# Kernel optimization log

Hardware: AMD Instinct MI355X
Metric: run time of the kernel (lower is better)

Reference implementation:

```python
import jax, jax.numpy as jnp
import numpy as np

D_MODEL = 1024
N_HEADS = 16
D_HEAD = D_MODEL // N_HEADS


def setup_inputs() -> dict:
    key = jax.random.key(0)
    ks = jax.random.split(key, 9)
    s = 1.0 / np.sqrt(D_MODEL)
    def lin(kw, kb):
        W = jax.random.uniform(kw, (D_MODEL, D_MODEL), jnp.float32, -s, s)
        b = jax.random.uniform(kb, (D_MODEL,), jnp.float32, -s, s)
        return W, b
    Wq, bq = lin(ks[0], ks[1])
    Wk, bk = lin(ks[2], ks[3])
    Wv, bv = lin(ks[4], ks[5])
    Wo, bo = lin(ks[6], ks[7])
    x = jax.random.normal(ks[8], (4, 2048, D_MODEL), jnp.float32)
    return {"x": x, "Wq": Wq, "bq": bq, "Wk": Wk, "bk": bk,
            "Wv": Wv, "bv": bv, "Wo": Wo, "bo": bo}


def reference(x, Wq, bq, Wk, bk, Wv, bv, Wo, bo):
    B, T, C = x.shape
    # torch Linear: y = x @ W.T + b
    Q = x @ Wq.T + bq
    K = x @ Wk.T + bk
    V = x @ Wv.T + bv
    # [B, H, T, Dh]
    Q = Q.reshape(B, T, N_HEADS, D_HEAD).transpose(0, 2, 1, 3)
    K = K.reshape(B, T, N_HEADS, D_HEAD).transpose(0, 2, 1, 3)
    V = V.reshape(B, T, N_HEADS, D_HEAD).transpose(0, 2, 1, 3)
    scale = jnp.float32(np.sqrt(D_HEAD))
    scores = jnp.einsum('bhqd,bhkd->bhqk', Q, K) / scale
    causal = jnp.tril(jnp.ones((T, T), dtype=bool))  # True where allowed
    scores = jnp.where(causal, scores, jnp.float32(-jnp.inf))
    attn = jax.nn.softmax(scores, axis=-1)
    out = jnp.einsum('bhqk,bhkd->bhqd', attn, V)
    out = out.transpose(0, 2, 1, 3).reshape(B, T, C)
    return out @ Wo.T + bo
```

## Files before the change

### kernel.cpp

```cpp
#include <hip/hip_runtime.h>
#include <hip/hip_bf16.h>


typedef float f32x4 __attribute__((ext_vector_type(4)));
typedef __bf16 bf16x8 __attribute__((ext_vector_type(8)));

#define DEVI __device__ __forceinline__

#define QSCALE 0.1803368801111204f

template<int N> struct IC { static constexpr int value = N; };

DEVI ushort f2b(float x) {
  __hip_bfloat16 h = __float2bfloat16(x);
  return __builtin_bit_cast(ushort, h);
}

DEVI unsigned int pkbf(float a, float b) {
#if __has_builtin(__builtin_amdgcn_cvt_pk_bf16_f32)
  typedef __bf16 bf16x2 __attribute__((ext_vector_type(2)));
  bf16x2 r = __builtin_amdgcn_cvt_pk_bf16_f32(a, b);
  return __builtin_bit_cast(unsigned int, r);
#else
  return (unsigned int)f2b(a) | ((unsigned int)f2b(b) << 16);
#endif
}

DEVI bf16x8 ldsFrag(const ushort* p) {
  return __builtin_bit_cast(bf16x8, *(const uint4*)p);
}

DEVI f32x4 mfma16(bf16x8 a, bf16x8 b, f32x4 c) {
  return __builtin_amdgcn_mfma_f32_16x16x32_bf16(a, b, c, 0, 0, 0);
}

DEVI void gload_lds16(const ushort* g, ushort* l) {
  __builtin_amdgcn_global_load_lds(
      (const __attribute__((address_space(1))) unsigned int*)g,
      (__attribute__((address_space(3))) unsigned int*)l, 16, 0, 0);
}

__global__ void k_cvt(const float4* __restrict__ in, ushort4* __restrict__ out, int n4) {
  int i = blockIdx.x * 256 + threadIdx.x;
  if (i >= n4) return;
  float4 f = in[i];
  ushort4 o;
  o.x = f2b(f.x); o.y = f2b(f.y); o.z = f2b(f.z); o.w = f2b(f.w);
  out[i] = o;
}

__global__ void k_cvtW(const float4* __restrict__ w0, const float4* __restrict__ w1,
                       const float4* __restrict__ w2, const float4* __restrict__ w3,
                       ushort4* __restrict__ out) {
  const int y = blockIdx.y;
  const float4* src = (y == 0) ? w0 : (y == 1) ? w1 : (y == 2) ? w2 : w3;
  const int i = blockIdx.x * 256 + threadIdx.x;
  float4 f = src[i];
  ushort4 o;
  o.x = f2b(f.x); o.y = f2b(f.y); o.z = f2b(f.z); o.w = f2b(f.w);
  out[y * 262144 + i] = o;
}

template<int MODE>
__global__ __launch_bounds__(256)
void k_gemm(const ushort* __restrict__ A, const ushort* __restrict__ W,
            const float* __restrict__ b0, const float* __restrict__ b1,
            const float* __restrict__ b2, float* __restrict__ outF,
            ushort* __restrict__ oQ, ushort* __restrict__ oK, ushort* __restrict__ oV) {
  __shared__ ushort As[128 * 64];
  __shared__ ushort Bs[128 * 64];
  const int tid = threadIdx.x;
  const int wave = tid >> 6, lane = tid & 63;
  const int col = lane & 15, quad = lane >> 4;
  const int id = blockIdx.x;
  const int s_ = id >> 3;
  const int m0 = ((id & 7) * 8 + (s_ & 7)) * 128;
  const int n0 = (s_ >> 3) * 128;
  const int wm = (wave >> 1) * 64, wn = (wave & 1) * 64;
  f32x4 acc[4][4] = {};

  const int grow = lane >> 3;
  const int gchunk = ((lane & 7) ^ grow) * 8;
  const ushort* Ag = A + (size_t)(m0 + wave * 8 + grow) * 1024 + gchunk;
  const ushort* Wg = W + (size_t)(n0 + wave * 8 + grow) * 1024 + gchunk;
  ushort* AsW = &As[wave * 512];
  ushort* BsW = &Bs[wave * 512];

  const int matId = (MODE == 0) ? (n0 >> 10) : 0;
  const int cswz = col & 7;

  auto kloop = [&](auto swc) {
    constexpr bool SW = (decltype(swc)::value != 0);
    for (int k0 = 0; k0 < 1024; k0 += 64) {
      __syncthreads();
#pragma unroll
      for (int g = 0; g < 4; ++g) {
        gload_lds16(Ag + (size_t)g * 32 * 1024 + k0, AsW + g * 2048);
        gload_lds16(Wg + (size_t)g * 32 * 1024 + k0, BsW + g * 2048);
      }
      __syncthreads();
#pragma unroll
      for (int kk = 0; kk < 2; ++kk) {
        bf16x8 af[4], bfr[4];
#pragma unroll
        for (int i = 0; i < 4; ++i)
          af[i] = ldsFrag(&As[(wm + i * 16 + col) * 64 + (((kk * 4 + quad) ^ cswz) * 8)]);
#pragma unroll
        for (int j = 0; j < 4; ++j)
          bfr[j] = ldsFrag(&Bs[(wn + j * 16 + col) * 64 + (((kk * 4 + quad) ^ cswz) * 8)]);
#pragma unroll
        for (int i = 0; i < 4; ++i)
#pragma unroll
          for (int j = 0; j < 4; ++j) {
            if constexpr (SW)
              acc[i][j] = mfma16(bfr[j], af[i], acc[i][j]);
            else
              acc[i][j] = mfma16(af[i], bfr[j], acc[i][j]);
          }
      }
    }
  };

  if (MODE == 1 || matId < 2) kloop(IC<1>{}); else kloop(IC<0>{});

  if (MODE == 1) {
#pragma unroll
    for (int j = 0; j < 4; ++j) {
      const int nb = n0 + wn + j * 16 + quad * 4;
      const float4 bb = *(const float4*)&b0[nb];
#pragma unroll
      for (int i = 0; i < 4; ++i) {
        const int m = m0 + wm + i * 16 + col;
        float4 v;
        v.x = acc[i][j][0] + bb.x;
        v.y = acc[i][j][1] + bb.y;
        v.z = acc[i][j][2] + bb.z;
        v.w = acc[i][j][3] + bb.w;
        *(float4*)&outF[(size_t)m * 1024 + nb] = v;
      }
    }
  } else if (matId < 2) {
    ushort* dst = (matId == 0) ? oQ : oK;
    const float* bias = (matId == 0) ? b0 : b1;
    const float sc = (matId == 0) ? QSCALE : 1.0f;
#pragma unroll
    for (int j = 0; j < 4; ++j) {
      const int nl = ((n0 & 1023) + wn + j * 16 + quad * 4);
      const int h = nl >> 6, dh0 = nl & 63;
      const float4 bb = *(const float4*)&bias[nl];
#pragma unroll
      for (int i = 0; i < 4; ++i) {
        const int m = m0 + wm + i * 16 + col;
        const int b = m >> 11, t = m & 2047;
        ushort4 pk;
        pk.x = f2b((acc[i][j][0] + bb.x) * sc);
        pk.y = f2b((acc[i][j][1] + bb.y) * sc);
        pk.z = f2b((acc[i][j][2] + bb.z) * sc);
        pk.w = f2b((acc[i][j][3] + bb.w) * sc);
        *(ushort4*)&dst[(((size_t)(b * 16 + h) * 2048) + t) * 64 + dh0] = pk;
      }
    }
  } else {
#pragma unroll
    for (int j = 0; j < 4; ++j) {
      const int nl = ((n0 & 1023) + wn + j * 16 + col);
      const int h = nl >> 6, dh = nl & 63;
      const float bn = b2[nl];
#pragma unroll
      for (int i = 0; i < 4; ++i) {
        const int mBase = m0 + wm + i * 16 + quad * 4;
        const int b = mBase >> 11, t = mBase & 2047;
        ushort4 pk;
        pk.x = f2b(acc[i][j][0] + bn);
        pk.y = f2b(acc[i][j][1] + bn);
        pk.z = f2b(acc[i][j][2] + bn);
        pk.w = f2b(acc[i][j][3] + bn);
        *(ushort4*)&oV[(((size_t)(b * 16 + h) * 64) + dh) * 2048 + t] = pk;
      }
    }
  }
}

__global__ __launch_bounds__(256, 3)
void k_attn(const ushort* __restrict__ Q, const ushort* __restrict__ K,
            const ushort* __restrict__ Vt, ushort* __restrict__ AO) {
  __shared__ ushort Ks[2 * 4096];
  __shared__ ushort Vs[2 * 4096];
  __shared__ ushort Os[512];
  __shared__ ushort Ps[4 * 2 * 16 * 72];
  const int tid = threadIdx.x;
  const int wave = tid >> 6, lane = tid & 63;
  const int col = lane & 15, quad = lane >> 4;
  const int id = blockIdx.x;
  const int bh = (id & 7) * 8 + ((id >> 3) & 7);
  const int tt = id >> 6;
  const int hi = tt >> 2, lo = tt & 3;
  const int t = (hi & 1) ? (15 - (hi >> 1) - 2 * lo) : ((hi >> 1) + 2 * lo);
  const int q0 = t * 128;
  const ushort* Qg = Q + (size_t)bh * 2048 * 64;
  const ushort* Kg = K + (size_t)bh * 2048 * 64;
  const ushort* Vg = Vt + (size_t)bh * 64 * 2048;

  if (tid < 128) {
    const ushort one = 0x3F80;
    ushort4 zv;
    if (tid < 8) { zv.x = one; zv.y = one; zv.z = one; zv.w = one; }
    else         { zv.x = 0;   zv.y = 0;   zv.z = 0;   zv.w = 0;   }
    *(ushort4*)&Os[tid * 4] = zv;
  }

  bf16x8 qf[2][2];
#pragma unroll
  for (int s = 0; s < 2; ++s) {
    const ushort* p = Qg + (q0 + wave * 32 + s * 16 + col) * 64 + quad * 8;
    qf[s][0] = __builtin_bit_cast(bf16x8, *(const uint4*)p);
    qf[s][1] = __builtin_bit_cast(bf16x8, *(const uint4*)(p + 32));
  }

  f32x4 o[2][4] = {};
  f32x4 la[2] = {};

  const int grow = lane >> 3;
  const int gchunk = ((lane & 7) ^ grow) * 8;
  const ushort* kPtr = Kg + (wave * 8 + grow) * 64 + gchunk;
  const ushort* vPtr = Vg + (size_t)(wave * 8 + grow) * 2048 + gchunk;
  ushort* Pw0 = &Ps[((wave * 2 + 0) * 16 + col) * 72];
  ushort* Pw1 = &Ps[((wave * 2 + 1) * 16 + col) * 72];
  const int cswz = col & 7;

  auto stage = [&](auto bufc) {
    constexpr int BUF = decltype(bufc)::value;
    ushort* kb = &Ks[BUF * 4096 + wave * 512];
    ushort* vb = &Vs[BUF * 4096 + wave * 512];
    gload_lds16(kPtr,             kb);
    gload_lds16(kPtr + 32 * 64,   kb + 2048);
    gload_lds16(vPtr,             vb);
    gload_lds16(vPtr + 32 * 2048, vb + 2048);
    kPtr += 64 * 64;
    vPtr += 64;
  };

  auto step = [&](auto bufc, auto maskc, int j0) {
    constexpr int BUF = decltype(bufc)::value;
    constexpr bool MASKED = (decltype(maskc)::value != 0);
    const ushort* Kb = &Ks[BUF * 4096];
    const ushort* Vb = &Vs[BUF * 4096];
    bf16x8 kf[4][2];
#pragma unroll
    for (int i = 0; i < 4; ++i) {
      kf[i][0] = ldsFrag(&Kb[(i * 16 + col) * 64 + (((0 * 4 + quad) ^ cswz) * 8)]);
      kf[i][1] = ldsFrag(&Kb[(i * 16 + col) * 64 + (((1 * 4 + quad) ^ cswz) * 8)]);
    }
#pragma unroll
    for (int s = 0; s < 2; ++s) {
      ushort* Pw = s ? Pw1 : Pw0;
      const int dlim = MASKED ? (q0 + wave * 32 + s * 16 + col - j0 - quad * 4) : 0;
#pragma unroll
      for (int i = 0; i < 4; ++i) {
        f32x4 z = {0.f, 0.f, 0.f, 0.f};
        f32x4 sv = mfma16(kf[i][0], qf[s][0], z);
        sv = mfma16(kf[i][1], qf[s][1], sv);
        if (MASKED) {
#pragma unroll
          for (int r = 0; r < 4; ++r)
            if (i * 16 + r > dlim) sv[r] = -1e30f;
        }
        f32x4 pv;
#pragma unroll
        for (int r = 0; r < 4; ++r) pv[r] = __builtin_amdgcn_exp2f(sv[r]);
        uint2 pk;
        pk.x = pkbf(pv[0], pv[1]);
        pk.y = pkbf(pv[2], pv[3]);
        *(uint2*)&Pw[i * 16 + quad * 4] = pk;
      }
    }
    bf16x8 osf = ldsFrag(&Os[col * 32 + quad * 8]);
#pragma unroll
    for (int c = 0; c < 2; ++c) {
      bf16x8 pb0 = ldsFrag(&Pw0[c * 32 + quad * 8]);
      bf16x8 pb1 = ldsFrag(&Pw1[c * 32 + quad * 8]);
      la[0] = mfma16(osf, pb0, la[0]);
      la[1] = mfma16(osf, pb1, la[1]);
#pragma unroll
      for (int i = 0; i < 4; ++i) {
        bf16x8 vf = ldsFrag(&Vb[(i * 16 + col) * 64 + (((c * 4 + quad) ^ cswz) * 8)]);
        o[0][i] = mfma16(vf, pb0, o[0][i]);
        o[1][i] = mfma16(vf, pb1, o[1][i]);
      }
    }
  };

  __syncthreads();
  stage(IC<0>{});
  for (int it2 = 0; it2 < t; ++it2) {
    __syncthreads();
    stage(IC<1>{});
    step(IC<0>{}, IC<0>{}, 0);
    __syncthreads();
    stage(IC<0>{});
    step(IC<1>{}, IC<0>{}, 0);
  }
  __syncthreads();
  stage(IC<1>{});
  step(IC<0>{}, IC<1>{}, q0);
  __syncthreads();
  step(IC<1>{}, IC<1>{}, q0 + 64);

  const float invs[2] = {1.0f / __shfl(la[0][0], col), 1.0f / __shfl(la[1][0], col)};
  const int b = bh >> 4, h = bh & 15;
#pragma unroll
  for (int s = 0; s < 2; ++s) {
    const float inv = invs[s];
    const int tq = q0 + wave * 32 + s * 16 + col;
    ushort* dst = AO + (size_t)(b * 2048 + tq) * 1024 + h * 64;
#pragma unroll
    for (int i = 0; i < 4; ++i) {
      f32x4 v = o[s][i];
      ushort4 pk;
      pk.x = f2b(v[0] * inv);
      pk.y = f2b(v[1] * inv);
      pk.z = f2b(v[2] * inv);
      pk.w = f2b(v[3] * inv);
      *(ushort4*)&dst[i * 16 + quad * 4] = pk;
    }
  }
}

extern "C" void kernel_launch(void* const* d_in, const int* in_sizes, int n_in,
                              void* d_out, int out_size, void* d_ws, size_t ws_size,
                              hipStream_t stream) {
  const float* x  = (const float*)d_in[0];
  const float* Wq = (const float*)d_in[1];
  const float* bq = (const float*)d_in[2];
  const float* Wk = (const float*)d_in[3];
  const float* bk = (const float*)d_in[4];
  const float* Wv = (const float*)d_in[5];
  const float* bv = (const float*)d_in[6];
  const float* Wo = (const float*)d_in[7];
  const float* bo = (const float*)d_in[8];
  float* out = (float*)d_out;

  char* ws = (char*)d_ws;
  ushort* xb    = (ushort*)ws;
  ushort* Wcat  = (ushort*)(ws + (size_t)16 * 1024 * 1024);
  ushort* Wob   = Wcat + (size_t)3 * 1024 * 1024;
  ushort* Qh    = (ushort*)(ws + (size_t)24 * 1024 * 1024);
  ushort* Kh    = Qh + (size_t)8192 * 1024;
  ushort* Vt    = Kh + (size_t)8192 * 1024;
  ushort* AO    = Vt + (size_t)8192 * 1024;

  k_cvt<<<8192, 256, 0, stream>>>((const float4*)x, (ushort4*)xb, 8192 * 1024 / 4);
  k_cvtW<<<dim3(1024, 4), 256, 0, stream>>>((const float4*)Wq, (const float4*)Wk,
                                            (const float4*)Wv, (const float4*)Wo,
                                            (ushort4*)Wcat);

  k_gemm<0><<<1536, 256, 0, stream>>>(xb, Wcat, bq, bk, bv, nullptr, Qh, Kh, Vt);

  k_attn<<<1024, 256, 0, stream>>>(Qh, Kh, Vt, AO);

  k_gemm<1><<<512, 256, 0, stream>>>(AO, Wob, bo, nullptr, nullptr, out,
                                     nullptr, nullptr, nullptr);
}
```

Baseline: 253.7 us.

## Use 512-thread attention blocks with paired causal tiles; merge conversion kernels

The attention kernel now uses 8 waves per block over 256-row query tiles. Each block processes a pair of tiles (t and 7-t) so causal work is balanced, and the grid drops to 256 blocks. The masked diagonal steps are gated per wave so waves skip fully masked K/V tiles. The x and weight float-to-bf16 conversions are merged into one launch to save a kernel launch. In exchange, occupancy falls to one block per CU and parallelism is coarser. Idle waves during diagonal steps and a 256-block grid on a chip with many CUs may hurt utilization.

```diff
diff --git a/kernel.cpp b/kernel.cpp
--- a/kernel.cpp
+++ b/kernel.cpp
@@ -40,25 +40,26 @@
       (__attribute__((address_space(3))) unsigned int*)l, 16, 0, 0);
 }
 
-__global__ void k_cvt(const float4* __restrict__ in, ushort4* __restrict__ out, int n4) {
-  int i = blockIdx.x * 256 + threadIdx.x;
-  if (i >= n4) return;
-  float4 f = in[i];
+__global__ void k_cvtAll(const float4* __restrict__ x,
+                         const float4* __restrict__ w0, const float4* __restrict__ w1,
+                         const float4* __restrict__ w2, const float4* __restrict__ w3,
+                         ushort4* __restrict__ xb, ushort4* __restrict__ wcat) {
+  const int blk = blockIdx.x;
+  const int i = blk * 256 + threadIdx.x;
+  float4 f;
+  ushort4* dst;
+  int di;
+  if (blk < 8192) {
+    f = x[i]; dst = xb; di = i;
+  } else {
+    const int wi = i - 8192 * 256;
+    const int sel = wi >> 18;
+    const float4* src = (sel == 0) ? w0 : (sel == 1) ? w1 : (sel == 2) ? w2 : w3;
+    f = src[wi & 262143]; dst = wcat; di = wi;
+  }
   ushort4 o;
   o.x = f2b(f.x); o.y = f2b(f.y); o.z = f2b(f.z); o.w = f2b(f.w);
-  out[i] = o;
-}
-
-__global__ void k_cvtW(const float4* __restrict__ w0, const float4* __restrict__ w1,
-                       const float4* __restrict__ w2, const float4* __restrict__ w3,
-                       ushort4* __restrict__ out) {
-  const int y = blockIdx.y;
-  const float4* src = (y == 0) ? w0 : (y == 1) ? w1 : (y == 2) ? w2 : w3;
-  const int i = blockIdx.x * 256 + threadIdx.x;
-  float4 f = src[i];
-  ushort4 o;
-  o.x = f2b(f.x); o.y = f2b(f.y); o.z = f2b(f.z); o.w = f2b(f.w);
-  out[y * 262144 + i] = o;
+  dst[di] = o;
 }
 
 template<int MODE>
@@ -181,22 +182,19 @@
   }
 }
 
-__global__ __launch_bounds__(256, 3)
+__global__ __launch_bounds__(512, 1)
 void k_attn(const ushort* __restrict__ Q, const ushort* __restrict__ K,
             const ushort* __restrict__ Vt, ushort* __restrict__ AO) {
   __shared__ ushort Ks[2 * 4096];
   __shared__ ushort Vs[2 * 4096];
   __shared__ ushort Os[512];
-  __shared__ ushort Ps[4 * 2 * 16 * 72];
+  __shared__ ushort Ps[16 * 16 * 72];
   const int tid = threadIdx.x;
   const int wave = tid >> 6, lane = tid & 63;
   const int col = lane & 15, quad = lane >> 4;
   const int id = blockIdx.x;
   const int bh = (id & 7) * 8 + ((id >> 3) & 7);
-  const int tt = id >> 6;
-  const int hi = tt >> 2, lo = tt & 3;
-  const int t = (hi & 1) ? (15 - (hi >> 1) - 2 * lo) : ((hi >> 1) + 2 * lo);
-  const int q0 = t * 128;
+  const int pr = id >> 6;
   const ushort* Qg = Q + (size_t)bh * 2048 * 64;
   const ushort* Kg = K + (size_t)bh * 2048 * 64;
   const ushort* Vg = Vt + (size_t)bh * 64 * 2048;
@@ -209,119 +207,127 @@
     *(ushort4*)&Os[tid * 4] = zv;
   }
 
-  bf16x8 qf[2][2];
-#pragma unroll
-  for (int s = 0; s < 2; ++s) {
-    const ushort* p = Qg + (q0 + wave * 32 + s * 16 + col) * 64 + quad * 8;
-    qf[s][0] = __builtin_bit_cast(bf16x8, *(const uint4*)p);
-    qf[s][1] = __builtin_bit_cast(bf16x8, *(const uint4*)(p + 32));
-  }
-
-  f32x4 o[2][4] = {};
-  f32x4 la[2] = {};
-
   const int grow = lane >> 3;
   const int gchunk = ((lane & 7) ^ grow) * 8;
-  const ushort* kPtr = Kg + (wave * 8 + grow) * 64 + gchunk;
-  const ushort* vPtr = Vg + (size_t)(wave * 8 + grow) * 2048 + gchunk;
+  const int cswz = col & 7;
   ushort* Pw0 = &Ps[((wave * 2 + 0) * 16 + col) * 72];
   ushort* Pw1 = &Ps[((wave * 2 + 1) * 16 + col) * 72];
-  const int cswz = col & 7;
-
-  auto stage = [&](auto bufc) {
-    constexpr int BUF = decltype(bufc)::value;
-    ushort* kb = &Ks[BUF * 4096 + wave * 512];
-    ushort* vb = &Vs[BUF * 4096 + wave * 512];
-    gload_lds16(kPtr,             kb);
-    gload_lds16(kPtr + 32 * 64,   kb + 2048);
-    gload_lds16(vPtr,             vb);
-    gload_lds16(vPtr + 32 * 2048, vb + 2048);
-    kPtr += 64 * 64;
-    vPtr += 64;
-  };
-
-  auto step = [&](auto bufc, auto maskc, int j0) {
-    constexpr int BUF = decltype(bufc)::value;
-    constexpr bool MASKED = (decltype(maskc)::value != 0);
-    const ushort* Kb = &Ks[BUF * 4096];
-    const ushort* Vb = &Vs[BUF * 4096];
-    bf16x8 kf[4][2];
-#pragma unroll
-    for (int i = 0; i < 4; ++i) {
-      kf[i][0] = ldsFrag(&Kb[(i * 16 + col) * 64 + (((0 * 4 + quad) ^ cswz) * 8)]);
-      kf[i][1] = ldsFrag(&Kb[(i * 16 + col) * 64 + (((1 * 4 + quad) ^ cswz) * 8)]);
-    }
+
+  for (int pp = 0; pp < 2; ++pp) {
+    const int t = pp ? (7 - pr) : pr;
+    const int q0 = t * 256;
+
+    bf16x8 qf[2][2];
 #pragma unroll
     for (int s = 0; s < 2; ++s) {
-      ushort* Pw = s ? Pw1 : Pw0;
-      const int dlim = MASKED ? (q0 + wave * 32 + s * 16 + col - j0 - quad * 4) : 0;
-#pragma unroll
-      for (int i = 0; i < 4; ++i) {
-        f32x4 z = {0.f, 0.f, 0.f, 0.f};
-        f32x4 sv = mfma16(kf[i][0], qf[s][0], z);
-        sv = mfma16(kf[i][1], qf[s][1], sv);
-        if (MASKED) {
-#pragma unroll
-          for (int r = 0; r < 4; ++r)
-            if (i * 16 + r > dlim) sv[r] = -1e30f;
+      const ushort* p = Qg + (q0 + wave * 32 + s * 16 + col) * 64 + quad * 8;
+      qf[s][0] = __builtin_bit_cast(bf16x8, *(const uint4*)p);
+      qf[s][1] = __builtin_bit_cast(bf16x8, *(const uint4*)(p + 32));
+    }
+
+    f32x4 o[2][4] = {};
+    f32x4 la[2] = {};
+
+    const ushort* kPtr = Kg + (wave * 8 + grow) * 64 + gchunk;
+    const ushort* vPtr = Vg + (size_t)(wave * 8 + grow) * 2048 + gchunk;
+
+    auto stage = [&](auto bufc) {
+      constexpr int BUF = decltype(bufc)::value;
+      gload_lds16(kPtr, &Ks[BUF * 4096 + wave * 512]);
+      gload_lds16(vPtr, &Vs[BUF * 4096 + wave * 512]);
+      kPtr += 64 * 64;
+      vPtr += 64;
+    };
+
+    auto step = [&](auto bufc, auto maskc, int j0) {
+      constexpr int BUF = decltype(bufc)::value;
+      constexpr bool MASKED = (decltype(maskc)::value != 0);
+      const ushort* Kb = &Ks[BUF * 4096];
+      const ushort* Vb = &Vs[BUF * 4096];
+      bf16x8 kf[4][2];
+#pragma unroll
+      for (int i = 0; i < 4; ++i) {
+        kf[i][0] = ldsFrag(&Kb[(i * 16 + col) * 64 + (((0 * 4 + quad) ^ cswz) * 8)]);
+        kf[i][1] = ldsFrag(&Kb[(i * 16 + col) * 64 + (((1 * 4 + quad) ^ cswz) * 8)]);
+      }
+#pragma unroll
+      for (int s = 0; s < 2; ++s) {
+        ushort* Pw = s ? Pw1 : Pw0;
+        const int dlim = MASKED ? (q0 + wave * 32 + s * 16 + col - j0 - quad * 4) : 0;
+#pragma unroll
+        for (int i = 0; i < 4; ++i) {
+          f32x4 z = {0.f, 0.f, 0.f, 0.f};
+          f32x4 sv = mfma16(kf[i][0], qf[s][0], z);
+          sv = mfma16(kf[i][1], qf[s][1], sv);
+          if (MASKED) {
+#pragma unroll
+            for (int r = 0; r < 4; ++r)
+              if (i * 16 + r > dlim) sv[r] = -1e30f;
+          }
+          f32x4 pv;
+#pragma unroll
+          for (int r = 0; r < 4; ++r) pv[r] = __builtin_amdgcn_exp2f(sv[r]);
+          uint2 pk;
+          pk.x = pkbf(pv[0], pv[1]);
+          pk.y = pkbf(pv[2], pv[3]);
+          *(uint2*)&Pw[i * 16 + quad * 4] = pk;
         }
-        f32x4 pv;
-#pragma unroll
-        for (int r = 0; r < 4; ++r) pv[r] = __builtin_amdgcn_exp2f(sv[r]);
-        uint2 pk;
-        pk.x = pkbf(pv[0], pv[1]);
-        pk.y = pkbf(pv[2], pv[3]);
-        *(uint2*)&Pw[i * 16 + quad * 4] = pk;
-      }
-    }
-    bf16x8 osf = ldsFrag(&Os[col * 32 + quad * 8]);
-#pragma unroll
-    for (int c = 0; c < 2; ++c) {
-      bf16x8 pb0 = ldsFrag(&Pw0[c * 32 + quad * 8]);
-      bf16x8 pb1 = ldsFrag(&Pw1[c * 32 + quad * 8]);
-      la[0] = mfma16(osf, pb0, la[0]);
-      la[1] = mfma16(osf, pb1, la[1]);
-#pragma unroll
-      for (int i = 0; i < 4; ++i) {
-        bf16x8 vf = ldsFrag(&Vb[(i * 16 + col) * 64 + (((c * 4 + quad) ^ cswz) * 8)]);
-        o[0][i] = mfma16(vf, pb0, o[0][i]);
-        o[1][i] = mfma16(vf, pb1, o[1][i]);
-      }
-    }
-  };
-
-  __syncthreads();
-  stage(IC<0>{});
-  for (int it2 = 0; it2 < t; ++it2) {
+      }
+      bf16x8 osf = ldsFrag(&Os[col * 32 + quad * 8]);
+#pragma unroll
+      for (int c = 0; c < 2; ++c) {
+        bf16x8 pb0 = ldsFrag(&Pw0[c * 32 + quad * 8]);
+        bf16x8 pb1 = ldsFrag(&Pw1[c * 32 + quad * 8]);
+        la[0] = mfma16(osf, pb0, la[0]);
+        la[1] = mfma16(osf, pb1, la[1]);
+#pragma unroll
+        for (int i = 0; i < 4; ++i) {
+          bf16x8 vf = ldsFrag(&Vb[(i * 16 + col) * 64 + (((c * 4 + quad) ^ cswz) * 8)]);
+          o[0][i] = mfma16(vf, pb0, o[0][i]);
+          o[1][i] = mfma16(vf, pb1, o[1][i]);
+        }
+      }
+    };
+
+    __syncthreads();
+    stage(IC<0>{});
+    for (int it2 = 0; it2 < 2 * t; ++it2) {
+      __syncthreads();
+      stage(IC<1>{});
+      step(IC<0>{}, IC<0>{}, 0);
+      __syncthreads();
+      stage(IC<0>{});
+      step(IC<1>{}, IC<0>{}, 0);
+    }
     __syncthreads();
     stage(IC<1>{});
-    step(IC<0>{}, IC<0>{}, 0);
+    step(IC<0>{}, IC<1>{}, q0);
     __syncthreads();
     stage(IC<0>{});
-    step(IC<1>{}, IC<0>{}, 0);
-  }
-  __syncthreads();
-  stage(IC<1>{});
-  step(IC<0>{}, IC<1>{}, q0);
-  __syncthreads();
-  step(IC<1>{}, IC<1>{}, q0 + 64);
-
-  const float invs[2] = {1.0f / __shfl(la[0][0], col), 1.0f / __shfl(la[1][0], col)};
-  const int b = bh >> 4, h = bh & 15;
-#pragma unroll
-  for (int s = 0; s < 2; ++s) {
-    const float inv = invs[s];
-    const int tq = q0 + wave * 32 + s * 16 + col;
-    ushort* dst = AO + (size_t)(b * 2048 + tq) * 1024 + h * 64;
-#pragma unroll
-    for (int i = 0; i < 4; ++i) {
-      f32x4 v = o[s][i];
-      ushort4 pk;
-      pk.x = f2b(v[0] * inv);
-      pk.y = f2b(v[1] * inv);
-      pk.z = f2b(v[2] * inv);
-      pk.w = f2b(v[3] * inv);
-      *(ushort4*)&dst[i * 16 + quad * 4] = pk;
+    if (wave >= 2) step(IC<1>{}, IC<1>{}, q0 + 64);
+    __syncthreads();
+    stage(IC<1>{});
+    if (wave >= 4) step(IC<0>{}, IC<1>{}, q0 + 128);
+    __syncthreads();
+    if (wave >= 6) step(IC<1>{}, IC<1>{}, q0 + 192);
+
+    const float invs[2] = {1.0f / __shfl(la[0][0], col), 1.0f / __shfl(la[1][0], col)};
+    const int b = bh >> 4, h = bh & 15;
+#pragma unroll
+    for (int s = 0; s < 2; ++s) {
+      const float inv = invs[s];
+      const int tq = q0 + wave * 32 + s * 16 + col;
+      ushort* dst = AO + (size_t)(b * 2048 + tq) * 1024 + h * 64;
+#pragma unroll
+      for (int i = 0; i < 4; ++i) {
+        f32x4 v = o[s][i];
+        ushort4 pk;
+        pk.x = f2b(v[0] * inv);
+        pk.y = f2b(v[1] * inv);
+        pk.z = f2b(v[2] * inv);
+        pk.w = f2b(v[3] * inv);
+        *(ushort4*)&dst[i * 16 + quad * 4] = pk;
+      }
     }
   }
 }
@@ -349,14 +355,14 @@
   ushort* Vt    = Kh + (size_t)8192 * 1024;
   ushort* AO    = Vt + (size_t)8192 * 1024;
 
-  k_cvt<<<8192, 256, 0, stream>>>((const float4*)x, (ushort4*)xb, 8192 * 1024 / 4);
-  k_cvtW<<<dim3(1024, 4), 256, 0, stream>>>((const float4*)Wq, (const float4*)Wk,
-                                            (const float4*)Wv, (const float4*)Wo,
-                                            (ushort4*)Wcat);
+  k_cvtAll<<<12288, 256, 0, stream>>>((const float4*)x,
+                                      (const float4*)Wq, (const float4*)Wk,
+                                      (const float4*)Wv, (const float4*)Wo,
+                                      (ushort4*)xb, (ushort4*)Wcat);
 
   k_gemm<0><<<1536, 256, 0, stream>>>(xb, Wcat, bq, bk, bv, nullptr, Qh, Kh, Vt);
 
-  k_attn<<<1024, 256, 0, stream>>>(Qh, Kh, Vt, AO);
+  k_attn<<<256, 512, 0, stream>>>(Qh, Kh, Vt, AO);
 
   k_gemm<1><<<512, 256, 0, stream>>>(AO, Wob, bo, nullptr, nullptr, out,
                                      nullptr, nullptr, nullptr);
```

After: 249.0 us. About the same (-1.8%).
